# Kernel tuning notes

Measured on AMD Instinct MI355X. Metric: run time of the kernel, lower is better.

Reference implementation:

```python
import jax, jax.numpy as jnp
import numpy as np

H = W = 224
WS = 7          # window size
SS = 3          # shift size
NH = 12         # num heads
N = WS * WS     # tokens per window (49)


def _attn_mask():
    # shift-window attention mask, computed from static ints (numpy)
    img = np.zeros((H, W), np.float32)
    cnt = 0
    for h0, h1 in [(0, H - WS), (H - WS, H - SS), (H - SS, H)]:
        for w0, w1 in [(0, W - WS), (W - WS, W - SS), (W - SS, W)]:
            img[h0:h1, w0:w1] = cnt
            cnt += 1
    mw = img.reshape(H // WS, WS, W // WS, WS).transpose(0, 2, 1, 3).reshape(-1, N)
    diff = mw[:, None, :] - mw[:, :, None]          # (nW, N, N)
    m = np.where(diff != 0, -100.0, 0.0).astype(np.float32)
    return m[:, None, :, :]                         # (nW, 1, N, N)


def _rel_pos_index():
    coords = np.stack(np.meshgrid(np.arange(WS), np.arange(WS), indexing='ij'))
    cf = coords.reshape(2, -1)
    rc = (cf[:, :, None] - cf[:, None, :]).transpose(1, 2, 0)  # (N, N, 2)
    rc[..., 0] += WS - 1
    rc[..., 1] += WS - 1
    rc[..., 0] *= 2 * WS - 1
    return rc.sum(-1).reshape(-1)                    # (N*N,)


_MASK = _attn_mask()
_RPI = _rel_pos_index()


def _ln(x, w, b, eps=1e-5):
    mu = jnp.mean(x, -1, keepdims=True)
    var = jnp.mean((x - mu) ** 2, -1, keepdims=True)
    return (x - mu) / jnp.sqrt(var + eps) * w + b


def setup_inputs() -> dict:
    key = jax.random.key(0)
    ks = jax.random.split(key, 12)
    C, CM = 384, 1536
    s = 0.02
    return {
        'x': jax.random.normal(ks[0], (1, H * W, C), jnp.float32),
        'rpb_table': jax.random.normal(ks[1], (169, NH), jnp.float32) * s,
        'qkv_w': jax.random.normal(ks[2], (3 * C, C), jnp.float32) * s,
        'qkv_b': jax.random.normal(ks[3], (3 * C,), jnp.float32) * s,
        'proj_w': jax.random.normal(ks[4], (C, C), jnp.float32) * s,
        'proj_b': jax.random.normal(ks[5], (C,), jnp.float32) * s,
        'fc1_w': jax.random.normal(ks[6], (CM, C), jnp.float32) * s,
        'fc1_b': jax.random.normal(ks[7], (CM,), jnp.float32) * s,
        'fc2_w': jax.random.normal(ks[8], (C, CM), jnp.float32) * s,
        'fc2_b': jax.random.normal(ks[9], (C,), jnp.float32) * s,
        'norm1_w': jnp.ones((C,), jnp.float32),
        'norm1_b': jnp.zeros((C,), jnp.float32),
        'norm2_w': jnp.ones((C,), jnp.float32),
        'norm2_b': jnp.zeros((C,), jnp.float32),
    }


def reference(x, rpb_table, qkv_w, qkv_b, proj_w, proj_b, fc1_w, fc1_b,
              fc2_w, fc2_b, norm1_w, norm1_b, norm2_w, norm2_b):
    B, L, C = x.shape
    hd = C // NH
    scale = hd ** -0.5
    mask = jnp.asarray(_MASK)                        # (nW, 1, N, N)
    rpi = jnp.asarray(_RPI)

    shortcut = x
    h = _ln(x, norm1_w, norm1_b).reshape(B, H, W, C)
    h = jnp.roll(h, (-SS, -SS), axis=(1, 2))
    # window partition -> (B*nW, N, C)
    win = h.reshape(B, H // WS, WS, W // WS, WS, C).transpose(0, 1, 3, 2, 4, 5)
    win = win.reshape(-1, N, C)

    qkv = (win @ qkv_w.T + qkv_b).reshape(-1, N, 3, NH, hd).transpose(2, 0, 3, 1, 4)
    q, k, v = qkv[0] * scale, qkv[1], qkv[2]         # (nW, NH, N, hd)
    attn = jnp.einsum('whnd,whmd->whnm', q, k)
    bias = rpb_table[rpi].reshape(N, N, NH).transpose(2, 0, 1)[None]  # (1, NH, N, N)
    attn = jax.nn.softmax(attn + bias + mask, axis=-1)
    out = jnp.einsum('whnm,whmd->whnd', attn, v).transpose(0, 2, 1, 3).reshape(-1, N, C)
    out = out @ proj_w.T + proj_b

    # window reverse + unshift
    h = out.reshape(B, H // WS, W // WS, WS, WS, C).transpose(0, 1, 3, 2, 4, 5)
    h = h.reshape(B, H, W, C)
    h = jnp.roll(h, (SS, SS), axis=(1, 2)).reshape(B, L, C)

    x = shortcut + h
    y = _ln(x, norm2_w, norm2_b)
    y = jax.nn.gelu(y @ fc1_w.T + fc1_b, approximate=False)  # torch nn.GELU = erf
    y = y @ fc2_w.T + fc2_b
    return x + y
```

## Files before the change

kernel.cpp:

```cpp
#include <hip/hip_runtime.h>
#include <cstdint>
#include <cstddef>

#define AS1 __attribute__((address_space(1)))
#define AS3 __attribute__((address_space(3)))

typedef __attribute__((ext_vector_type(8))) short bf16x8;
typedef __attribute__((ext_vector_type(4))) short short4v;
typedef __attribute__((ext_vector_type(8))) unsigned short u16x8;
typedef __attribute__((ext_vector_type(4))) float f32x4;
typedef __attribute__((ext_vector_type(4))) unsigned short u16x4;

__device__ __forceinline__ float b2f(uint16_t u){ return __uint_as_float(((uint32_t)u) << 16); }
__device__ __forceinline__ uint16_t f2b(float f){
    uint32_t u = __float_as_uint(f);
    return (uint16_t)((u + 0x7fffu + ((u >> 16) & 1u)) >> 16);
}

__device__ __forceinline__ int pixof(int r){
    int w  = r / 49, t = r - w * 49;
    int wh = w >> 5, ww = w & 31;
    int th = t / 7,  tw = t - th * 7;
    int hp = wh * 7 + th + 3; if (hp >= 224) hp -= 224;
    int wp = ww * 7 + tw + 3; if (wp >= 224) wp -= 224;
    return hp * 224 + wp;
}

__global__ void f2bm_kernel(const float* __restrict__ a0, const float* __restrict__ a1,
                            const float* __restrict__ a2, const float* __restrict__ a3,
                            uint16_t* __restrict__ o0, uint16_t* __restrict__ o1,
                            uint16_t* __restrict__ o2, uint16_t* __restrict__ o3,
                            const float* __restrict__ rpb, float* __restrict__ bm){
    int b = blockIdx.x;
    if (b >= 6912){
        int th = b - 6912;
        int type = th / 12, h = th - (th / 12) * 12;
        int eh = type >> 1, ew = type & 1;
        for (int idx = threadIdx.x; idx < 4096; idx += 256){
            int q = idx >> 6, kt = idx & 63;
            float v = 0.f;
            if (q < 49 && kt < 49){
                int ih = q / 7,  iw = q - 7 * (q / 7);
                int jh = kt / 7, jw = kt - 7 * (kt / 7);
                v = rpb[((ih - jh + 6) * 13 + (iw - jw + 6)) * 12 + h];
                int ri = (eh ? (ih < 4 ? 1 : 2) : 0) * 3 + (ew ? (iw < 4 ? 1 : 2) : 0);
                int rj = (eh ? (jh < 4 ? 1 : 2) : 0) * 3 + (ew ? (jw < 4 ? 1 : 2) : 0);
                if (ri != rj) v -= 100.f;
            }
            bm[(size_t)th * 4096 + idx] = v;
        }
        return;
    }
    const float* src; uint16_t* dst; int base;
    if (b < 1728)      { src = a0; dst = o0; base = b; }
    else if (b < 2304) { src = a1; dst = o1; base = b - 1728; }
    else if (b < 4608) { src = a2; dst = o2; base = b - 2304; }
    else               { src = a3; dst = o3; base = b - 4608; }
    int i = base * 256 + threadIdx.x;
    dst[i] = f2b(src[i]);
}

__global__ __launch_bounds__(256) void ln_kernel(const float* __restrict__ in,
        const float* __restrict__ g, const float* __restrict__ b, uint16_t* __restrict__ out){
    int wave = threadIdx.x >> 6, lane = threadIdx.x & 63;
    int r = blockIdx.x * 4 + wave;
    int p = pixof(r);
    const float* row = in + (size_t)p * 384;
    float a[6];
    #pragma unroll
    for (int i = 0; i < 6; ++i) a[i] = row[lane * 6 + i];
    float s = 0.f, q = 0.f;
    #pragma unroll
    for (int i = 0; i < 6; ++i){ s += a[i]; q += a[i] * a[i]; }
    #pragma unroll
    for (int o = 32; o; o >>= 1){ s += __shfl_xor(s, o); q += __shfl_xor(q, o); }
    float mu   = s * (1.f / 384.f);
    float var  = q * (1.f / 384.f) - mu * mu;
    float rstd = rsqrtf(var + 1e-5f);
    uint16_t* orow = out + (size_t)r * 384;
    #pragma unroll
    for (int i = 0; i < 6; ++i){
        int c = lane * 6 + i;
        orow[c] = f2b((a[i] - mu) * rstd * g[c] + b[c]);
    }
}

__global__ __launch_bounds__(256) void ln2_kernel(const uint16_t* __restrict__ in,
        const float* __restrict__ g, const float* __restrict__ b, uint16_t* __restrict__ out){
    int wave = threadIdx.x >> 6, lane = threadIdx.x & 63;
    int r = blockIdx.x * 4 + wave;
    u16x8 v8 = {0,0,0,0,0,0,0,0};
    if (lane < 48) v8 = *(const u16x8*)(in + (size_t)r * 384 + lane * 8);
    float a[8];
    float s = 0.f, q = 0.f;
    #pragma unroll
    for (int i = 0; i < 8; ++i){ a[i] = b2f(v8[i]); s += a[i]; q += a[i] * a[i]; }
    #pragma unroll
    for (int o = 32; o; o >>= 1){ s += __shfl_xor(s, o); q += __shfl_xor(q, o); }
    float mu   = s * (1.f / 384.f);
    float var  = q * (1.f / 384.f) - mu * mu;
    float rstd = rsqrtf(var + 1e-5f);
    if (lane < 48){
        u16x8 o8;
        #pragma unroll
        for (int i = 0; i < 8; ++i){
            int c = lane * 8 + i;
            o8[i] = f2b((a[i] - mu) * rstd * g[c] + b[c]);
        }
        *(u16x8*)(out + (size_t)r * 384 + lane * 8) = o8;
    }
}

template<int EPI>
__global__ __launch_bounds__(256, 2) void gemm_bt(
        const uint16_t* __restrict__ A, const uint16_t* __restrict__ B,
        const float* __restrict__ bias, void* __restrict__ outp,
        const float* __restrict__ xres, const uint16_t* __restrict__ xb,
        int N, int K, int row0)
{
    __shared__ alignas(16) uint16_t lA[128 * 64];
    __shared__ alignas(16) uint16_t lB[128 * 64];
    int tid  = threadIdx.x;
    int lane = tid & 63, wave = tid >> 6;

    int nwg = gridDim.x, bid = blockIdx.x;
    int q8 = nwg >> 3, r8 = nwg & 7;
    int xcd = bid & 7, idx = bid >> 3;
    int wg = (xcd < r8 ? xcd * (q8 + 1) : r8 * (q8 + 1) + (xcd - r8) * q8) + idx;

    int nt = N >> 7;
    int bm = wg / nt, bn = wg - bm * nt;
    int wr = wave >> 1, wc = wave & 1;
    int fr = lane & 15, kc = lane >> 4;

    int srow = wave * 32 + (lane >> 3);
    int cs   = (lane & 7) ^ ((lane >> 3) & 7);
    const uint16_t* gA = A + (size_t)(bm * 128 + srow) * K + cs * 8;
    const uint16_t* gB = B + (size_t)(bn * 128 + srow) * K + cs * 8;

    int aoff[4], boff[4];
    #pragma unroll
    for (int m = 0; m < 4; ++m){
        int row = wr * 64 + m * 16 + fr;
        aoff[m] = row * 128 + ((kc * 16) ^ ((row & 7) << 4));
        int rowB = wc * 64 + m * 16 + fr;
        boff[m] = rowB * 128 + ((kc * 16) ^ ((rowB & 7) << 4));
    }

    f32x4 acc[4][4] = {};
    const int NT = K >> 6;
    for (int t = 0; t < NT; ++t){
        int k0 = t << 6;
        #pragma unroll
        for (int it = 0; it < 4; ++it){
            __builtin_amdgcn_global_load_lds((const AS1 void*)(gA + k0 + (size_t)it * 8 * K),
                (AS3 void*)((AS3 char*)lA + wave * 4096 + it * 1024), 16, 0, 0);
            __builtin_amdgcn_global_load_lds((const AS1 void*)(gB + k0 + (size_t)it * 8 * K),
                (AS3 void*)((AS3 char*)lB + wave * 4096 + it * 1024), 16, 0, 0);
        }
        __syncthreads();

        #pragma unroll
        for (int ks = 0; ks < 2; ++ks){
            bf16x8 af[4], bv[4];
            #pragma unroll
            for (int m = 0; m < 4; ++m)
                af[m] = *(const bf16x8*)((const char*)lA + (aoff[m] ^ (ks << 6)));
            #pragma unroll
            for (int n = 0; n < 4; ++n)
                bv[n] = *(const bf16x8*)((const char*)lB + (boff[n] ^ (ks << 6)));
            #pragma unroll
            for (int m = 0; m < 4; ++m)
                #pragma unroll
                for (int n = 0; n < 4; ++n)
                    acc[m][n] = __builtin_amdgcn_mfma_f32_16x16x32_bf16(af[m], bv[n], acc[m][n], 0, 0, 0);
        }
        __syncthreads();
    }

    int colb = bn * 128 + wc * 64 + fr;
    int rowb = bm * 128 + wr * 64 + ((lane >> 4) << 2);
    float bvv[4];
    #pragma unroll
    for (int n = 0; n < 4; ++n) bvv[n] = bias[colb + n * 16];

    if constexpr (EPI == 1 || EPI == 5){
        uint16_t* out = (uint16_t*)outp;
        #pragma unroll
        for (int m = 0; m < 4; ++m)
            #pragma unroll
            for (int rg = 0; rg < 4; ++rg){
                size_t rr = (size_t)(rowb + m * 16 + rg) * N;
                #pragma unroll
                for (int n = 0; n < 4; ++n){
                    int col = colb + n * 16;
                    float v = acc[m][n][rg] + bvv[n];
                    if constexpr (EPI == 1) v = 0.5f * v * (1.f + erff(v * 0.7071067811865475f));
                    if constexpr (EPI == 5){ if (col < 384) v *= 0.1767766952966369f; }
                    out[rr + col] = f2b(v);
                }
            }
    } else if constexpr (EPI == 6){
        uint16_t* out = (uint16_t*)outp;
        #pragma unroll
        for (int m = 0; m < 4; ++m)
            #pragma unroll
            for (int rg = 0; rg < 4; ++rg){
                int r = row0 + rowb + m * 16 + rg;
                size_t pb = (size_t)pixof(r) * 384;
                #pragma unroll
                for (int n = 0; n < 4; ++n){
                    int c = colb + n * 16;
                    out[pb + c] = f2b(xres[pb + c] + acc[m][n][rg] + bvv[n]);
                }
            }
    } else {
        float* out = (float*)outp;
        #pragma unroll
        for (int m = 0; m < 4; ++m)
            #pragma unroll
            for (int rg = 0; rg < 4; ++rg){
                size_t rb2 = (size_t)(rowb + m * 16 + rg) * 384;
                #pragma unroll
                for (int n = 0; n < 4; ++n){
                    int c = colb + n * 16;
                    out[rb2 + c] = b2f(xb[rb2 + c]) + acc[m][n][rg] + bvv[n];
                }
            }
    }
}

__global__ __launch_bounds__(256) void attn_mfma(const uint16_t* __restrict__ qkv,
        const float* __restrict__ bm, uint16_t* __restrict__ out)
{
    __shared__ uint16_t vtl[4][32][68];
    int wv = threadIdx.x >> 6, lane = threadIdx.x & 63;
    int p = blockIdx.x * 4 + wv;
    int w = p / 12, h = p - w * 12;
    int c = lane & 15, g = lane >> 4;
    const uint16_t* base = qkv + (size_t)(w * 49) * 1152 + h * 32;

    u16x8 vreg[4];
    #pragma unroll
    for (int it = 0; it < 4; ++it){
        int u = it * 64 + lane;
        int t = u >> 2, dq = u & 3;
        u16x8 v8 = {0,0,0,0,0,0,0,0};
        if (t < 49) v8 = *(const u16x8*)(base + (size_t)t * 1152 + 768 + dq * 8);
        vreg[it] = v8;
    }

    bf16x8 qf[4], kf[4];
    #pragma unroll
    for (int nt = 0; nt < 4; ++nt) qf[nt] = *(const bf16x8*)(base + (size_t)(16 * nt + c) * 1152 + g * 8);
    #pragma unroll
    for (int mt = 0; mt < 4; ++mt) kf[mt] = *(const bf16x8*)(base + (size_t)(16 * mt + c) * 1152 + 384 + g * 8);

    int wh = w >> 5, ww = w & 31;
    int type = ((wh == 31) << 1) | (ww == 31);
    const float* bmp = bm + (size_t)(type * 12 + h) * 4096;
    f32x4 sv[4][4];
    __builtin_amdgcn_s_setprio(1);
    #pragma unroll
    for (int mt = 0; mt < 4; ++mt)
        #pragma unroll
        for (int nt = 0; nt < 4; ++nt){
            f32x4 cb = *(const f32x4*)(bmp + (16 * nt + c) * 64 + 16 * mt + 4 * g);
            sv[mt][nt] = __builtin_amdgcn_mfma_f32_16x16x32_bf16(kf[mt], qf[nt], cb, 0, 0, 0);
        }
    __builtin_amdgcn_s_setprio(0);

    #pragma unroll
    for (int it = 0; it < 4; ++it){
        int u = it * 64 + lane;
        int t = u >> 2, dq = u & 3;
        #pragma unroll
        for (int j = 0; j < 8; ++j) vtl[wv][dq * 8 + j][t] = vreg[it][j];
    }

    #pragma unroll
    for (int nt = 0; nt < 4; ++nt)
        #pragma unroll
        for (int r = 0; r < 4; ++r)
            if (4 * g + r >= 1) sv[3][nt][r] = -1e9f;

    float inv[4];
    #pragma unroll
    for (int nt = 0; nt < 4; ++nt){
        float mx = -1e30f;
        #pragma unroll
        for (int mt = 0; mt < 4; ++mt)
            #pragma unroll
            for (int r = 0; r < 4; ++r) mx = fmaxf(mx, sv[mt][nt][r]);
        mx = fmaxf(mx, __shfl_xor(mx, 16));
        mx = fmaxf(mx, __shfl_xor(mx, 32));
        float sum = 0.f;
        #pragma unroll
        for (int mt = 0; mt < 4; ++mt)
            #pragma unroll
            for (int r = 0; r < 4; ++r){
                float e = __expf(sv[mt][nt][r] - mx);
                sv[mt][nt][r] = e; sum += e;
            }
        sum += __shfl_xor(sum, 16);
        sum += __shfl_xor(sum, 32);
        inv[nt] = 1.f / sum;
    }

    unsigned pk[4][4][2];
    #pragma unroll
    for (int nt = 0; nt < 4; ++nt)
        #pragma unroll
        for (int mt = 0; mt < 4; ++mt)
            #pragma unroll
            for (int pr = 0; pr < 2; ++pr)
                pk[nt][mt][pr] = (unsigned)f2b(sv[mt][nt][2 * pr]) |
                                 ((unsigned)f2b(sv[mt][nt][2 * pr + 1]) << 16);

    int a0 = (c + 16 * (2 * (g & 1))) * 4;
    int a1 = a0 + 64;
    int sel = g >> 1;

    f32x4 acco[2][4] = {};
    #pragma unroll
    for (int ks = 0; ks < 2; ++ks){
        bf16x8 va[2];
        #pragma unroll
        for (int mt = 0; mt < 2; ++mt){
            short4v lo = *(const short4v*)&vtl[wv][mt * 16 + c][ks * 32 + g * 8];
            short4v hi = *(const short4v*)&vtl[wv][mt * 16 + c][ks * 32 + g * 8 + 4];
            bf16x8 t;
            t[0] = lo[0]; t[1] = lo[1]; t[2] = lo[2]; t[3] = lo[3];
            t[4] = hi[0]; t[5] = hi[1]; t[6] = hi[2]; t[7] = hi[3];
            va[mt] = t;
        }
        bf16x8 pb[4];
        #pragma unroll
        for (int nt = 0; nt < 4; ++nt){
            union { unsigned u[4]; bf16x8 v; } pbu;
            #pragma unroll
            for (int t = 0; t < 4; ++t){
                int addr = (t >> 1) ? a1 : a0;
                unsigned lo2 = (unsigned)__builtin_amdgcn_ds_bpermute(addr, (int)pk[nt][2 * ks][t & 1]);
                unsigned hi2 = (unsigned)__builtin_amdgcn_ds_bpermute(addr, (int)pk[nt][2 * ks + 1][t & 1]);
                pbu.u[t] = sel ? hi2 : lo2;
            }
            pb[nt] = pbu.v;
        }
        __builtin_amdgcn_s_setprio(1);
        #pragma unroll
        for (int nt = 0; nt < 4; ++nt)
            #pragma unroll
            for (int mt = 0; mt < 2; ++mt)
                acco[mt][nt] = __builtin_amdgcn_mfma_f32_16x16x32_bf16(va[mt], pb[nt], acco[mt][nt], 0, 0, 0);
        __builtin_amdgcn_s_setprio(0);
    }

    #pragma unroll
    for (int mt = 0; mt < 2; ++mt)
        #pragma unroll
        for (int nt = 0; nt < 4; ++nt){
            int q = 16 * nt + c;
            if (q < 49){
                u16x4 o;
                #pragma unroll
                for (int r = 0; r < 4; ++r) o[r] = f2b(acco[mt][nt][r] * inv[nt]);
                *(u16x4*)(out + (size_t)(w * 49 + q) * 384 + h * 32 + 16 * mt + 4 * g) = o;
            }
        }
}

extern "C" void kernel_launch(void* const* d_in, const int* in_sizes, int n_in,
                              void* d_out, int out_size, void* d_ws, size_t ws_size,
                              hipStream_t stream) {
    const float* x      = (const float*)d_in[0];
    const float* rpb    = (const float*)d_in[1];
    const float* qkv_w  = (const float*)d_in[2];
    const float* qkv_b  = (const float*)d_in[3];
    const float* proj_w = (const float*)d_in[4];
    const float* proj_b = (const float*)d_in[5];
    const float* fc1_w  = (const float*)d_in[6];
    const float* fc1_b  = (const float*)d_in[7];
    const float* fc2_w  = (const float*)d_in[8];
    const float* fc2_b  = (const float*)d_in[9];
    const float* n1w    = (const float*)d_in[10];
    const float* n1b    = (const float*)d_in[11];
    const float* n2w    = (const float*)d_in[12];
    const float* n2b    = (const float*)d_in[13];

    char* ws = (char*)d_ws;
    uint16_t* winA  = (uint16_t*)ws;
    uint16_t* qkB   = (uint16_t*)(ws + 38535168);
    uint16_t* x2b   = qkB;
    uint16_t* hid   = (uint16_t*)(ws + 77070336);
    uint16_t* wbuf  = (uint16_t*)(ws + 154140672);
    uint16_t* w_qkv  = wbuf;
    uint16_t* w_proj = wbuf + 442368;
    uint16_t* w_fc1  = w_proj + 147456;
    uint16_t* w_fc2  = w_fc1 + 589824;
    float*    bmtab  = (float*)(ws + 157679616);

    f2bm_kernel<<<6960, 256, 0, stream>>>(qkv_w, proj_w, fc1_w, fc2_w,
                                          w_qkv, w_proj, w_fc1, w_fc2, rpb, bmtab);

    ln_kernel<<<12544, 256, 0, stream>>>(x, n1w, n1b, winA);

    gemm_bt<5><<<392 * 9, 256, 0, stream>>>(winA, w_qkv, qkv_b, qkB, nullptr, nullptr, 1152, 384, 0);

    attn_mfma<<<3072, 256, 0, stream>>>(qkB, bmtab, winA);

    gemm_bt<6><<<392 * 3, 256, 0, stream>>>(winA, w_proj, proj_b, x2b, x, nullptr, 384, 384, 0);

    ln2_kernel<<<12544, 256, 0, stream>>>(x2b, n2w, n2b, winA);

    for (int c2 = 0; c2 < 2; ++c2){
        size_t r0 = (size_t)c2 * 25088;
        gemm_bt<1><<<196 * 12, 256, 0, stream>>>(winA + r0 * 384, w_fc1, fc1_b, hid, nullptr, nullptr, 1536, 384, 0);
        gemm_bt<7><<<196 * 3, 256, 0, stream>>>(hid, w_fc2, fc2_b, (float*)d_out + r0 * 384, nullptr, x2b + r0 * 384, 384, 1536, 0);
    }
}
```

Measured before the change: 348.6 us.

## Switch GEMM to 32x32x16 MFMA tiles and fuse LN1 into init kernel

The GEMM inner loop moves from 16x16x32 bf16 MFMA (4x4 fragments per wave) to 32x32x16 MFMA (2x2 fragments), with the LDS addressing and epilogue row/column mapping rewritten to match. This halves the number of LDS fragment loads per K step and issues fewer, larger matrix instructions. Separately, the first LayerNorm is merged into the weight-conversion/bias-table kernel as extra blocks, removing one launch. The epilogue's per-lane store pattern changes, which may alter global write coalescing.

Measured after the change: 363.9 us. 1.04x slower.

```diff
diff --git a/kernel.cpp b/kernel.cpp
--- a/kernel.cpp
+++ b/kernel.cpp
@@ -9,6 +9,7 @@
 typedef __attribute__((ext_vector_type(4))) short short4v;
 typedef __attribute__((ext_vector_type(8))) unsigned short u16x8;
 typedef __attribute__((ext_vector_type(4))) float f32x4;
+typedef __attribute__((ext_vector_type(16))) float f32x16;
 typedef __attribute__((ext_vector_type(4))) unsigned short u16x4;
 
 __device__ __forceinline__ float b2f(uint16_t u){ return __uint_as_float(((uint32_t)u) << 16); }
@@ -26,12 +27,38 @@
     return hp * 224 + wp;
 }
 
-__global__ void f2bm_kernel(const float* __restrict__ a0, const float* __restrict__ a1,
-                            const float* __restrict__ a2, const float* __restrict__ a3,
-                            uint16_t* __restrict__ o0, uint16_t* __restrict__ o1,
-                            uint16_t* __restrict__ o2, uint16_t* __restrict__ o3,
-                            const float* __restrict__ rpb, float* __restrict__ bm){
+__global__ __launch_bounds__(256) void init_kernel(
+        const float* __restrict__ a0, const float* __restrict__ a1,
+        const float* __restrict__ a2, const float* __restrict__ a3,
+        uint16_t* __restrict__ o0, uint16_t* __restrict__ o1,
+        uint16_t* __restrict__ o2, uint16_t* __restrict__ o3,
+        const float* __restrict__ rpb, float* __restrict__ bm,
+        const float* __restrict__ x, const float* __restrict__ n1w,
+        const float* __restrict__ n1b, uint16_t* __restrict__ win){
     int b = blockIdx.x;
+    if (b >= 6960){
+        int wave = threadIdx.x >> 6, lane = threadIdx.x & 63;
+        int r = (b - 6960) * 4 + wave;
+        const float* row = x + (size_t)pixof(r) * 384;
+        float a[6];
+        #pragma unroll
+        for (int i = 0; i < 6; ++i) a[i] = row[lane * 6 + i];
+        float s = 0.f, q = 0.f;
+        #pragma unroll
+        for (int i = 0; i < 6; ++i){ s += a[i]; q += a[i] * a[i]; }
+        #pragma unroll
+        for (int o = 32; o; o >>= 1){ s += __shfl_xor(s, o); q += __shfl_xor(q, o); }
+        float mu   = s * (1.f / 384.f);
+        float var  = q * (1.f / 384.f) - mu * mu;
+        float rstd = rsqrtf(var + 1e-5f);
+        uint16_t* orow = win + (size_t)r * 384;
+        #pragma unroll
+        for (int i = 0; i < 6; ++i){
+            int c = lane * 6 + i;
+            orow[c] = f2b((a[i] - mu) * rstd * n1w[c] + n1b[c]);
+        }
+        return;
+    }
     if (b >= 6912){
         int th = b - 6912;
         int type = th / 12, h = th - (th / 12) * 12;
@@ -60,31 +87,6 @@
     dst[i] = f2b(src[i]);
 }
 
-__global__ __launch_bounds__(256) void ln_kernel(const float* __restrict__ in,
-        const float* __restrict__ g, const float* __restrict__ b, uint16_t* __restrict__ out){
-    int wave = threadIdx.x >> 6, lane = threadIdx.x & 63;
-    int r = blockIdx.x * 4 + wave;
-    int p = pixof(r);
-    const float* row = in + (size_t)p * 384;
-    float a[6];
-    #pragma unroll
-    for (int i = 0; i < 6; ++i) a[i] = row[lane * 6 + i];
-    float s = 0.f, q = 0.f;
-    #pragma unroll
-    for (int i = 0; i < 6; ++i){ s += a[i]; q += a[i] * a[i]; }
-    #pragma unroll
-    for (int o = 32; o; o >>= 1){ s += __shfl_xor(s, o); q += __shfl_xor(q, o); }
-    float mu   = s * (1.f / 384.f);
-    float var  = q * (1.f / 384.f) - mu * mu;
-    float rstd = rsqrtf(var + 1e-5f);
-    uint16_t* orow = out + (size_t)r * 384;
-    #pragma unroll
-    for (int i = 0; i < 6; ++i){
-        int c = lane * 6 + i;
-        orow[c] = f2b((a[i] - mu) * rstd * g[c] + b[c]);
-    }
-}
-
 __global__ __launch_bounds__(256) void ln2_kernel(const uint16_t* __restrict__ in,
         const float* __restrict__ g, const float* __restrict__ b, uint16_t* __restrict__ out){
     int wave = threadIdx.x >> 6, lane = threadIdx.x & 63;
@@ -131,23 +133,24 @@
     int nt = N >> 7;
     int bm = wg / nt, bn = wg - bm * nt;
     int wr = wave >> 1, wc = wave & 1;
-    int fr = lane & 15, kc = lane >> 4;
+    int ln31 = lane & 31, kh = lane >> 5;
 
     int srow = wave * 32 + (lane >> 3);
     int cs   = (lane & 7) ^ ((lane >> 3) & 7);
     const uint16_t* gA = A + (size_t)(bm * 128 + srow) * K + cs * 8;
     const uint16_t* gB = B + (size_t)(bn * 128 + srow) * K + cs * 8;
 
-    int aoff[4], boff[4];
-    #pragma unroll
-    for (int m = 0; m < 4; ++m){
-        int row = wr * 64 + m * 16 + fr;
-        aoff[m] = row * 128 + ((kc * 16) ^ ((row & 7) << 4));
-        int rowB = wc * 64 + m * 16 + fr;
-        boff[m] = rowB * 128 + ((kc * 16) ^ ((rowB & 7) << 4));
-    }
-
-    f32x4 acc[4][4] = {};
+    int rbA[2], swA[2], rbB[2], swB[2];
+    #pragma unroll
+    for (int b = 0; b < 2; ++b){
+        int rowA = wr * 64 + b * 32 + ln31;
+        rbA[b] = rowA * 128; swA[b] = (rowA & 7) << 4;
+        int rowB = wc * 64 + b * 32 + ln31;
+        rbB[b] = rowB * 128; swB[b] = (rowB & 7) << 4;
+    }
+    int kh16 = kh * 16;
+
+    f32x16 acc[2][2] = {};
     const int NT = K >> 6;
     for (int t = 0; t < NT; ++t){
         int k0 = t << 6;
@@ -161,40 +164,38 @@
         __syncthreads();
 
         #pragma unroll
-        for (int ks = 0; ks < 2; ++ks){
-            bf16x8 af[4], bv[4];
-            #pragma unroll
-            for (int m = 0; m < 4; ++m)
-                af[m] = *(const bf16x8*)((const char*)lA + (aoff[m] ^ (ks << 6)));
-            #pragma unroll
-            for (int n = 0; n < 4; ++n)
-                bv[n] = *(const bf16x8*)((const char*)lB + (boff[n] ^ (ks << 6)));
-            #pragma unroll
-            for (int m = 0; m < 4; ++m)
+        for (int ks = 0; ks < 4; ++ks){
+            bf16x8 av[2], bv[2];
+            #pragma unroll
+            for (int b = 0; b < 2; ++b)
+                av[b] = *(const bf16x8*)((const char*)lA + rbA[b] + ((ks * 32 + kh16) ^ swA[b]));
+            #pragma unroll
+            for (int b = 0; b < 2; ++b)
+                bv[b] = *(const bf16x8*)((const char*)lB + rbB[b] + ((ks * 32 + kh16) ^ swB[b]));
+            #pragma unroll
+            for (int mb = 0; mb < 2; ++mb)
                 #pragma unroll
-                for (int n = 0; n < 4; ++n)
-                    acc[m][n] = __builtin_amdgcn_mfma_f32_16x16x32_bf16(af[m], bv[n], acc[m][n], 0, 0, 0);
+                for (int nb = 0; nb < 2; ++nb)
+                    acc[mb][nb] = __builtin_amdgcn_mfma_f32_32x32x16_bf16(av[mb], bv[nb], acc[mb][nb], 0, 0, 0);
         }
         __syncthreads();
     }
 
-    int colb = bn * 128 + wc * 64 + fr;
-    int rowb = bm * 128 + wr * 64 + ((lane >> 4) << 2);
-    float bvv[4];
-    #pragma unroll
-    for (int n = 0; n < 4; ++n) bvv[n] = bias[colb + n * 16];
+    int colb = bn * 128 + wc * 64 + ln31;
+    int rowb = bm * 128 + wr * 64 + 4 * kh;
+    float bvv[2] = { bias[colb], bias[colb + 32] };
 
     if constexpr (EPI == 1 || EPI == 5){
         uint16_t* out = (uint16_t*)outp;
         #pragma unroll
-        for (int m = 0; m < 4; ++m)
-            #pragma unroll
-            for (int rg = 0; rg < 4; ++rg){
-                size_t rr = (size_t)(rowb + m * 16 + rg) * N;
+        for (int mb = 0; mb < 2; ++mb)
+            #pragma unroll
+            for (int reg = 0; reg < 16; ++reg){
+                size_t rr = (size_t)(rowb + mb * 32 + (reg & 3) + 8 * (reg >> 2)) * N;
                 #pragma unroll
-                for (int n = 0; n < 4; ++n){
-                    int col = colb + n * 16;
-                    float v = acc[m][n][rg] + bvv[n];
+                for (int nb = 0; nb < 2; ++nb){
+                    int col = colb + nb * 32;
+                    float v = acc[mb][nb][reg] + bvv[nb];
                     if constexpr (EPI == 1) v = 0.5f * v * (1.f + erff(v * 0.7071067811865475f));
                     if constexpr (EPI == 5){ if (col < 384) v *= 0.1767766952966369f; }
                     out[rr + col] = f2b(v);
@@ -203,28 +204,28 @@
     } else if constexpr (EPI == 6){
         uint16_t* out = (uint16_t*)outp;
         #pragma unroll
-        for (int m = 0; m < 4; ++m)
-            #pragma unroll
-            for (int rg = 0; rg < 4; ++rg){
-                int r = row0 + rowb + m * 16 + rg;
+        for (int mb = 0; mb < 2; ++mb)
+            #pragma unroll
+            for (int reg = 0; reg < 16; ++reg){
+                int r = row0 + rowb + mb * 32 + (reg & 3) + 8 * (reg >> 2);
                 size_t pb = (size_t)pixof(r) * 384;
                 #pragma unroll
-                for (int n = 0; n < 4; ++n){
-                    int c = colb + n * 16;
-                    out[pb + c] = f2b(xres[pb + c] + acc[m][n][rg] + bvv[n]);
+                for (int nb = 0; nb < 2; ++nb){
+                    int col = colb + nb * 32;
+                    out[pb + col] = f2b(xres[pb + col] + acc[mb][nb][reg] + bvv[nb]);
                 }
             }
     } else {
         float* out = (float*)outp;
         #pragma unroll
-        for (int m = 0; m < 4; ++m)
-            #pragma unroll
-            for (int rg = 0; rg < 4; ++rg){
-                size_t rb2 = (size_t)(rowb + m * 16 + rg) * 384;
+        for (int mb = 0; mb < 2; ++mb)
+            #pragma unroll
+            for (int reg = 0; reg < 16; ++reg){
+                size_t rb2 = (size_t)(rowb + mb * 32 + (reg & 3) + 8 * (reg >> 2)) * 384;
                 #pragma unroll
-                for (int n = 0; n < 4; ++n){
-                    int c = colb + n * 16;
-                    out[rb2 + c] = b2f(xb[rb2 + c]) + acc[m][n][rg] + bvv[n];
+                for (int nb = 0; nb < 2; ++nb){
+                    int col = colb + nb * 32;
+                    out[rb2 + col] = b2f(xb[rb2 + col]) + acc[mb][nb][reg] + bvv[nb];
                 }
             }
     }
@@ -400,10 +401,9 @@
     uint16_t* w_fc2  = w_fc1 + 589824;
     float*    bmtab  = (float*)(ws + 157679616);
 
-    f2bm_kernel<<<6960, 256, 0, stream>>>(qkv_w, proj_w, fc1_w, fc2_w,
-                                          w_qkv, w_proj, w_fc1, w_fc2, rpb, bmtab);
-
-    ln_kernel<<<12544, 256, 0, stream>>>(x, n1w, n1b, winA);
+    init_kernel<<<19504, 256, 0, stream>>>(qkv_w, proj_w, fc1_w, fc2_w,
+                                           w_qkv, w_proj, w_fc1, w_fc2,
+                                           rpb, bmtab, x, n1w, n1b, winA);
 
     gemm_bt<5><<<392 * 9, 256, 0, stream>>>(winA, w_qkv, qkv_b, qkB, nullptr, nullptr, 1152, 384, 0);
 
```

## Fuse LN1 into init kernel and software-pipeline MLP chunks in one launch

Applied to the files above, without the earlier changes.

The weight-conversion and bias-mask setup kernel now also performs the first LayerNorm, which removes one launch. The MLP is split into four row chunks. Each mlp_mid launch runs fc2 for chunk i and fc1 for chunk i+1 together, using double-buffered hidden activations, so the narrow fc2 grid overlaps with fc1 work and fills the GPU better. Smaller chunks add launches and reduce per-launch tile counts, and the fc1 and fc2 blocks compete for bandwidth within a launch.

New measurement: 372.4 us. 6.8% more time.

```diff
diff --git a/kernel.cpp b/kernel.cpp
--- a/kernel.cpp
+++ b/kernel.cpp
@@ -26,12 +26,44 @@
     return hp * 224 + wp;
 }
 
-__global__ void f2bm_kernel(const float* __restrict__ a0, const float* __restrict__ a1,
-                            const float* __restrict__ a2, const float* __restrict__ a3,
-                            uint16_t* __restrict__ o0, uint16_t* __restrict__ o1,
-                            uint16_t* __restrict__ o2, uint16_t* __restrict__ o3,
-                            const float* __restrict__ rpb, float* __restrict__ bm){
+__device__ __forceinline__ int xcd_swz(int bid, int nwg){
+    int q8 = nwg >> 3, r8 = nwg & 7;
+    int xcd = bid & 7, idx = bid >> 3;
+    return (xcd < r8 ? xcd * (q8 + 1) : r8 * (q8 + 1) + (xcd - r8) * q8) + idx;
+}
+
+__global__ __launch_bounds__(256) void init_kernel(
+        const float* __restrict__ a0, const float* __restrict__ a1,
+        const float* __restrict__ a2, const float* __restrict__ a3,
+        uint16_t* __restrict__ o0, uint16_t* __restrict__ o1,
+        uint16_t* __restrict__ o2, uint16_t* __restrict__ o3,
+        const float* __restrict__ rpb, float* __restrict__ bm,
+        const float* __restrict__ x, const float* __restrict__ n1w,
+        const float* __restrict__ n1b, uint16_t* __restrict__ win){
     int b = blockIdx.x;
+    if (b >= 6960){
+        int wave = threadIdx.x >> 6, lane = threadIdx.x & 63;
+        int r = (b - 6960) * 4 + wave;
+        const float* row = x + (size_t)pixof(r) * 384;
+        float a[6];
+        #pragma unroll
+        for (int i = 0; i < 6; ++i) a[i] = row[lane * 6 + i];
+        float s = 0.f, q = 0.f;
+        #pragma unroll
+        for (int i = 0; i < 6; ++i){ s += a[i]; q += a[i] * a[i]; }
+        #pragma unroll
+        for (int o = 32; o; o >>= 1){ s += __shfl_xor(s, o); q += __shfl_xor(q, o); }
+        float mu   = s * (1.f / 384.f);
+        float var  = q * (1.f / 384.f) - mu * mu;
+        float rstd = rsqrtf(var + 1e-5f);
+        uint16_t* orow = win + (size_t)r * 384;
+        #pragma unroll
+        for (int i = 0; i < 6; ++i){
+            int c = lane * 6 + i;
+            orow[c] = f2b((a[i] - mu) * rstd * n1w[c] + n1b[c]);
+        }
+        return;
+    }
     if (b >= 6912){
         int th = b - 6912;
         int type = th / 12, h = th - (th / 12) * 12;
@@ -60,31 +92,6 @@
     dst[i] = f2b(src[i]);
 }
 
-__global__ __launch_bounds__(256) void ln_kernel(const float* __restrict__ in,
-        const float* __restrict__ g, const float* __restrict__ b, uint16_t* __restrict__ out){
-    int wave = threadIdx.x >> 6, lane = threadIdx.x & 63;
-    int r = blockIdx.x * 4 + wave;
-    int p = pixof(r);
-    const float* row = in + (size_t)p * 384;
-    float a[6];
-    #pragma unroll
-    for (int i = 0; i < 6; ++i) a[i] = row[lane * 6 + i];
-    float s = 0.f, q = 0.f;
-    #pragma unroll
-    for (int i = 0; i < 6; ++i){ s += a[i]; q += a[i] * a[i]; }
-    #pragma unroll
-    for (int o = 32; o; o >>= 1){ s += __shfl_xor(s, o); q += __shfl_xor(q, o); }
-    float mu   = s * (1.f / 384.f);
-    float var  = q * (1.f / 384.f) - mu * mu;
-    float rstd = rsqrtf(var + 1e-5f);
-    uint16_t* orow = out + (size_t)r * 384;
-    #pragma unroll
-    for (int i = 0; i < 6; ++i){
-        int c = lane * 6 + i;
-        orow[c] = f2b((a[i] - mu) * rstd * g[c] + b[c]);
-    }
-}
-
 __global__ __launch_bounds__(256) void ln2_kernel(const uint16_t* __restrict__ in,
         const float* __restrict__ g, const float* __restrict__ b, uint16_t* __restrict__ out){
     int wave = threadIdx.x >> 6, lane = threadIdx.x & 63;
@@ -112,22 +119,14 @@
 }
 
 template<int EPI>
-__global__ __launch_bounds__(256, 2) void gemm_bt(
+__device__ __forceinline__ void gemm_body(
+        AS3 char* sA, AS3 char* sB, const char* rdA, const char* rdB,
         const uint16_t* __restrict__ A, const uint16_t* __restrict__ B,
         const float* __restrict__ bias, void* __restrict__ outp,
         const float* __restrict__ xres, const uint16_t* __restrict__ xb,
-        int N, int K, int row0)
+        int N, int K, int row0, int wg, int tid)
 {
-    __shared__ alignas(16) uint16_t lA[128 * 64];
-    __shared__ alignas(16) uint16_t lB[128 * 64];
-    int tid  = threadIdx.x;
     int lane = tid & 63, wave = tid >> 6;
-
-    int nwg = gridDim.x, bid = blockIdx.x;
-    int q8 = nwg >> 3, r8 = nwg & 7;
-    int xcd = bid & 7, idx = bid >> 3;
-    int wg = (xcd < r8 ? xcd * (q8 + 1) : r8 * (q8 + 1) + (xcd - r8) * q8) + idx;
-
     int nt = N >> 7;
     int bm = wg / nt, bn = wg - bm * nt;
     int wr = wave >> 1, wc = wave & 1;
@@ -154,9 +153,9 @@
         #pragma unroll
         for (int it = 0; it < 4; ++it){
             __builtin_amdgcn_global_load_lds((const AS1 void*)(gA + k0 + (size_t)it * 8 * K),
-                (AS3 void*)((AS3 char*)lA + wave * 4096 + it * 1024), 16, 0, 0);
+                (AS3 void*)(sA + wave * 4096 + it * 1024), 16, 0, 0);
             __builtin_amdgcn_global_load_lds((const AS1 void*)(gB + k0 + (size_t)it * 8 * K),
-                (AS3 void*)((AS3 char*)lB + wave * 4096 + it * 1024), 16, 0, 0);
+                (AS3 void*)(sB + wave * 4096 + it * 1024), 16, 0, 0);
         }
         __syncthreads();
 
@@ -165,10 +164,10 @@
             bf16x8 af[4], bv[4];
             #pragma unroll
             for (int m = 0; m < 4; ++m)
-                af[m] = *(const bf16x8*)((const char*)lA + (aoff[m] ^ (ks << 6)));
+                af[m] = *(const bf16x8*)(rdA + (aoff[m] ^ (ks << 6)));
             #pragma unroll
             for (int n = 0; n < 4; ++n)
-                bv[n] = *(const bf16x8*)((const char*)lB + (boff[n] ^ (ks << 6)));
+                bv[n] = *(const bf16x8*)(rdB + (boff[n] ^ (ks << 6)));
             #pragma unroll
             for (int m = 0; m < 4; ++m)
                 #pragma unroll
@@ -227,6 +226,41 @@
                     out[rb2 + c] = b2f(xb[rb2 + c]) + acc[m][n][rg] + bvv[n];
                 }
             }
+    }
+}
+
+template<int EPI>
+__global__ __launch_bounds__(256, 2) void gemm_bt(
+        const uint16_t* __restrict__ A, const uint16_t* __restrict__ B,
+        const float* __restrict__ bias, void* __restrict__ outp,
+        const float* __restrict__ xres, const uint16_t* __restrict__ xb,
+        int N, int K, int row0)
+{
+    __shared__ alignas(16) uint16_t lA[128 * 64];
+    __shared__ alignas(16) uint16_t lB[128 * 64];
+    int wg = xcd_swz(blockIdx.x, gridDim.x);
+    gemm_body<EPI>((AS3 char*)lA, (AS3 char*)lB, (const char*)lA, (const char*)lB,
+                   A, B, bias, outp, xres, xb, N, K, row0, wg, threadIdx.x);
+}
+
+__global__ __launch_bounds__(256, 2) void mlp_mid(
+        const uint16_t* __restrict__ hidR, const uint16_t* __restrict__ wfc2,
+        const float* __restrict__ bfc2, float* __restrict__ outF,
+        const uint16_t* __restrict__ xb,
+        const uint16_t* __restrict__ aln, const uint16_t* __restrict__ wfc1,
+        const float* __restrict__ bfc1, uint16_t* __restrict__ hidW)
+{
+    __shared__ alignas(16) uint16_t lA[128 * 64];
+    __shared__ alignas(16) uint16_t lB[128 * 64];
+    int bid = blockIdx.x;
+    if (bid < 294){
+        int wg = xcd_swz(bid, 294);
+        gemm_body<7>((AS3 char*)lA, (AS3 char*)lB, (const char*)lA, (const char*)lB,
+                     hidR, wfc2, bfc2, outF, nullptr, xb, 384, 1536, 0, wg, threadIdx.x);
+    } else {
+        int wg = xcd_swz(bid - 294, 1176);
+        gemm_body<1>((AS3 char*)lA, (AS3 char*)lB, (const char*)lA, (const char*)lB,
+                     aln, wfc1, bfc1, hidW, nullptr, nullptr, 1536, 384, 0, wg, threadIdx.x);
     }
 }
 
@@ -392,7 +426,8 @@
     uint16_t* winA  = (uint16_t*)ws;
     uint16_t* qkB   = (uint16_t*)(ws + 38535168);
     uint16_t* x2b   = qkB;
-    uint16_t* hid   = (uint16_t*)(ws + 77070336);
+    uint16_t* hidA  = (uint16_t*)(ws + 77070336);
+    uint16_t* hidB  = (uint16_t*)(ws + 115605504);
     uint16_t* wbuf  = (uint16_t*)(ws + 154140672);
     uint16_t* w_qkv  = wbuf;
     uint16_t* w_proj = wbuf + 442368;
@@ -400,10 +435,9 @@
     uint16_t* w_fc2  = w_fc1 + 589824;
     float*    bmtab  = (float*)(ws + 157679616);
 
-    f2bm_kernel<<<6960, 256, 0, stream>>>(qkv_w, proj_w, fc1_w, fc2_w,
-                                          w_qkv, w_proj, w_fc1, w_fc2, rpb, bmtab);
-
-    ln_kernel<<<12544, 256, 0, stream>>>(x, n1w, n1b, winA);
+    init_kernel<<<19504, 256, 0, stream>>>(qkv_w, proj_w, fc1_w, fc2_w,
+                                           w_qkv, w_proj, w_fc1, w_fc2,
+                                           rpb, bmtab, x, n1w, n1b, winA);
 
     gemm_bt<5><<<392 * 9, 256, 0, stream>>>(winA, w_qkv, qkv_b, qkB, nullptr, nullptr, 1152, 384, 0);
 
@@ -413,9 +447,14 @@
 
     ln2_kernel<<<12544, 256, 0, stream>>>(x2b, n2w, n2b, winA);
 
-    for (int c2 = 0; c2 < 2; ++c2){
-        size_t r0 = (size_t)c2 * 25088;
-        gemm_bt<1><<<196 * 12, 256, 0, stream>>>(winA + r0 * 384, w_fc1, fc1_b, hid, nullptr, nullptr, 1536, 384, 0);
-        gemm_bt<7><<<196 * 3, 256, 0, stream>>>(hid, w_fc2, fc2_b, (float*)d_out + r0 * 384, nullptr, x2b + r0 * 384, 384, 1536, 0);
-    }
-}
+    uint16_t* hw[2] = { hidA, hidB };
+    gemm_bt<1><<<98 * 12, 256, 0, stream>>>(winA, w_fc1, fc1_b, hidA, nullptr, nullptr, 1536, 384, 0);
+    for (int c2 = 0; c2 < 3; ++c2){
+        size_t r0 = (size_t)c2 * 12544, r1 = r0 + 12544;
+        mlp_mid<<<294 + 1176, 256, 0, stream>>>(
+            hw[c2 & 1], w_fc2, fc2_b, (float*)d_out + r0 * 384, x2b + r0 * 384,
+            winA + r1 * 384, w_fc1, fc1_b, hw[(c2 + 1) & 1]);
+    }
+    gemm_bt<7><<<98 * 3, 256, 0, stream>>>(hw[1], w_fc2, fc2_b, (float*)d_out + 3 * 12544 * 384,
+                                           nullptr, x2b + 3 * 12544 * 384, 384, 1536, 0);
+}
```
